# Optimization experiments

Measured on AMD Instinct MI355X. Metric: run time of the kernel, lower is better.

The kernel has to match this reference:

```python
import jax, jax.numpy as jnp
import numpy as np


def setup_inputs() -> dict:
    key = jax.random.key(0)
    k1, k2 = jax.random.split(key)
    B, N, M, D = 4, 8192, 8192, 3
    pred_points = jax.random.normal(k1, (B, N, D), dtype=jnp.float32)
    gt_points = jax.random.normal(k2, (B, M, D), dtype=jnp.float32)
    return {"pred_points": pred_points, "gt_points": gt_points}


def reference(pred_points, gt_points):
    p2 = jnp.sum(pred_points * pred_points, axis=-1)  # [B, N]
    g2 = jnp.sum(gt_points * gt_points, axis=-1)      # [B, M]
    cross = jnp.einsum("bnd,bmd->bnm", pred_points, gt_points)  # [B, N, M]
    d2 = p2[:, :, None] + g2[:, None, :] - 2.0 * cross
    dist = jnp.sqrt(jnp.maximum(d2, 0.0))             # [B, N, M]
    min_pred_to_gt = jnp.min(dist, axis=-1)           # [B, N]
    min_gt_to_pred = jnp.min(dist, axis=-2)           # [B, M]
    return min_pred_to_gt.mean() + min_gt_to_pred.mean()
```

## Files before the change

### kernel.cpp

```cpp
#include <hip/hip_runtime.h>


#define B_ 4
#define N_ 8192
#define TM 1024
#define SM (N_ / TM)
#define THREADS 512
#define CSN 8

__device__ __forceinline__ float min3f(float a, float b, float c) {
  float d;
  asm("v_min3_f32 %0, %1, %2, %3" : "=v"(d) : "v"(a), "v"(b), "v"(c));
  return d;
}

template<int RC>
__global__ __launch_bounds__(THREADS) void chamfer_sym(
    const float* __restrict__ pred, const float* __restrict__ gt,
    float* __restrict__ rowpart, float* __restrict__ colpart,
    float* __restrict__ accws) {
  constexpr int TN = RC * 64;
  constexpr int SN = N_ / TN;
  __shared__ float4 mlds[TM];
  __shared__ float sbuf[4096];

  const int b  = blockIdx.z;
  const int tn = blockIdx.y;
  const int tm = blockIdx.x;
  const int tid = threadIdx.x;
  const int i = tid & 15;
  const int j = tid >> 4;

  if (tm == 0 && tn == 0 && b == 0 && tid == 0) {
    atomicExch(&accws[0], 0.0f);
    atomicExch(((unsigned int*)accws) + 1, 0u);
  }

  const float* qsrc = pred + (size_t)b * N_ * 3;
  const float* tsrc = gt   + (size_t)b * N_ * 3;

  if (tid < 256) {
    const float* tb = tsrc + (size_t)tm * TM * 3;
    const int p0 = tid * 4;
    const float4 f0 = *(const float4*)(tb + 3 * p0);
    const float4 f1 = *(const float4*)(tb + 3 * p0 + 4);
    const float4 f2 = *(const float4*)(tb + 3 * p0 + 8);
    mlds[p0+0] = make_float4(f0.x,f0.y,f0.z, fmaf(f0.x,f0.x,fmaf(f0.y,f0.y,f0.z*f0.z)));
    mlds[p0+1] = make_float4(f0.w,f1.x,f1.y, fmaf(f0.w,f0.w,fmaf(f1.x,f1.x,f1.y*f1.y)));
    mlds[p0+2] = make_float4(f1.z,f1.w,f2.x, fmaf(f1.z,f1.z,fmaf(f1.w,f1.w,f2.x*f2.x)));
    mlds[p0+3] = make_float4(f2.y,f2.z,f2.w, fmaf(f2.y,f2.y,fmaf(f2.z,f2.z,f2.w*f2.w)));
  }

  float colacc[32];
#pragma unroll
  for (int c = 0; c < 32; ++c) colacc[c] = 3.4e38f;

  __syncthreads();

  const int nbase = tn * TN;

  for (int rc = 0; rc < RC; ++rc) {
    const float* qb = qsrc + (size_t)(nbase + rc * 64 + i * 4) * 3;
    const float4 g0 = *(const float4*)(qb);
    const float4 g1 = *(const float4*)(qb + 4);
    const float4 g2 = *(const float4*)(qb + 8);
    const float qx[4] = {g0.x, g0.w, g1.z, g2.y};
    const float qy[4] = {g0.y, g1.x, g1.w, g2.z};
    const float qz[4] = {g0.z, g1.y, g2.x, g2.w};
    float nx[4], ny[4], nz[4], q2[4], racc[4];
#pragma unroll
    for (int r = 0; r < 4; ++r) {
      nx[r] = -2.0f * qx[r]; ny[r] = -2.0f * qy[r]; nz[r] = -2.0f * qz[r];
      q2[r] = fmaf(qx[r],qx[r], fmaf(qy[r],qy[r], qz[r]*qz[r]));
      racc[r] = 3.4e38f;
    }

#pragma unroll
    for (int cs = 0; cs < CSN; ++cs) {
      const int mb = cs * 128 + j * 4;
      const float4 t0 = mlds[mb+0];
      const float4 t1 = mlds[mb+1];
      const float4 t2 = mlds[mb+2];
      const float4 t3 = mlds[mb+3];
      float s[4][4];
#pragma unroll
      for (int r = 0; r < 4; ++r) {
        s[r][0] = fmaf(nx[r],t0.x, fmaf(ny[r],t0.y, fmaf(nz[r],t0.z, t0.w)));
        s[r][1] = fmaf(nx[r],t1.x, fmaf(ny[r],t1.y, fmaf(nz[r],t1.z, t1.w)));
        s[r][2] = fmaf(nx[r],t2.x, fmaf(ny[r],t2.y, fmaf(nz[r],t2.z, t2.w)));
        s[r][3] = fmaf(nx[r],t3.x, fmaf(ny[r],t3.y, fmaf(nz[r],t3.z, t3.w)));
        racc[r] = min3f(racc[r], s[r][0], s[r][1]);
        racc[r] = min3f(racc[r], s[r][2], s[r][3]);
      }
#pragma unroll
      for (int c = 0; c < 4; ++c) {
        colacc[cs*4+c] = min3f(colacc[cs*4+c], s[0][c] + q2[0], s[1][c] + q2[1]);
        colacc[cs*4+c] = min3f(colacc[cs*4+c], s[2][c] + q2[2], s[3][c] + q2[3]);
      }
    }

    const int buf = (rc & 1) * 2048;
#pragma unroll
    for (int r = 0; r < 4; ++r) sbuf[buf + j*64 + i*4 + r] = racc[r] + q2[r];
    __syncthreads();
    {
      const int row = tid >> 3, g = tid & 7;
      const float v0 = sbuf[buf + (g*4+0)*64 + row];
      const float v1 = sbuf[buf + (g*4+1)*64 + row];
      const float v2 = sbuf[buf + (g*4+2)*64 + row];
      const float v3 = sbuf[buf + (g*4+3)*64 + row];
      float v = fminf(min3f(v0, v1, v2), v3);
      v = fminf(v, __shfl_xor(v, 1, 64));
      v = fminf(v, __shfl_xor(v, 2, 64));
      v = fminf(v, __shfl_xor(v, 4, 64));
      if (g == 0)
        rowpart[((size_t)b * SM + tm) * N_ + nbase + rc*64 + row] = v;
    }
  }

  __syncthreads();
#pragma unroll
  for (int p = 0; p < 4; ++p) {
#pragma unroll
    for (int k = 0; k < 8; ++k) {
      sbuf[i*256 + (k>>2)*128 + j*4 + (k&3)] = colacc[(2*p + (k>>2))*4 + (k&3)];
    }
    __syncthreads();
    if (tid < 256) {
      float v = sbuf[tid];
#pragma unroll
      for (int ii = 1; ii <= 13; ii += 2)
        v = min3f(v, sbuf[ii*256 + tid], sbuf[(ii+1)*256 + tid]);
      v = fminf(v, sbuf[15*256 + tid]);
      colpart[((size_t)b * SN + tn) * N_ + tm*TM + p*256 + tid] = v;
    }
    __syncthreads();
  }
}

template<int SN>
__global__ __launch_bounds__(256) void chamfer_fin(
    const float* __restrict__ rowpart, const float* __restrict__ colpart,
    float* __restrict__ accws, float* __restrict__ out) {
  const int t = blockIdx.x * 256 + threadIdx.x;
  const int b = t >> 13;
  const int n = t & (N_ - 1);
  float v = rowpart[(size_t)(b * SM) * N_ + n];
#pragma unroll
  for (int s = 1; s < SM; ++s) v = fminf(v, rowpart[(size_t)(b*SM + s) * N_ + n]);
  float sum = sqrtf(fmaxf(v, 0.0f));
  float w = colpart[(size_t)(b * SN) * N_ + n];
#pragma unroll
  for (int s = 1; s < SN; ++s) w = fminf(w, colpart[(size_t)(b*SN + s) * N_ + n]);
  sum += sqrtf(fmaxf(w, 0.0f));
#pragma unroll
  for (int off = 32; off > 0; off >>= 1) sum += __shfl_down(sum, off, 64);
  __shared__ float ws4[4];
  const int lane = threadIdx.x & 63, wid = threadIdx.x >> 6;
  if (lane == 0) ws4[wid] = sum;
  __syncthreads();
  if (threadIdx.x == 0) {
    const float bs = (ws4[0] + ws4[1]) + (ws4[2] + ws4[3]);
    atomicAdd(&accws[0], bs);
    __threadfence();
    const unsigned old = atomicAdd(((unsigned int*)accws) + 1, 1u);
    if (old == gridDim.x - 1) {
      __threadfence();
      const float tot = atomicAdd(&accws[0], 0.0f);
      out[0] = tot * (1.0f / 32768.0f);
    }
  }
}

extern "C" void kernel_launch(void* const* d_in, const int* in_sizes, int n_in,
                              void* d_out, int out_size, void* d_ws, size_t ws_size,
                              hipStream_t stream) {
  const float* pred = (const float*)d_in[0];
  const float* gt   = (const float*)d_in[1];
  float* out = (float*)d_out;
  float* rowpart = (float*)d_ws;
  const size_t rowfl = (size_t)B_ * SM * N_;
  const size_t base = rowfl * sizeof(float) + 64;

#define LAUNCH(RCV)                                                            \
  {                                                                            \
    constexpr int SNV = N_ / (RCV * 64);                                       \
    float* colpart = rowpart + rowfl;                                          \
    float* accws = colpart + (size_t)B_ * SNV * N_;                            \
    chamfer_sym<RCV><<<dim3(SM, SNV, B_), THREADS, 0, stream>>>(               \
        pred, gt, rowpart, colpart, accws);                                    \
    chamfer_fin<SNV><<<128, 256, 0, stream>>>(rowpart, colpart, accws, out);   \
  }

  if      (ws_size >= base + (size_t)B_ * 8 * N_ * sizeof(float)) LAUNCH(16)
  else if (ws_size >= base + (size_t)B_ * 4 * N_ * sizeof(float)) LAUNCH(32)
  else if (ws_size >= base + (size_t)B_ * 2 * N_ * sizeof(float)) LAUNCH(64)
  else                                                            LAUNCH(128)
#undef LAUNCH
}
```

Baseline: 103.2 us.

## Restructure chamfer kernel with wave-shuffle row reduction and LDS atomicMin column merge

Remaps threads so each wave's 32 lanes cover the column tile, letting row minima be reduced with xor shuffles instead of a shared-memory transpose and extra barriers per row chunk. Column minima are merged with LDS atomicMin on non-negative float bit patterns rather than a multi-pass shared buffer reduction. The mlds layout is XOR-swizzled to avoid bank conflicts, launch bounds are raised to four blocks, RC becomes a runtime parameter with smaller values (more blocks) when workspace allows, and the finisher splits row and column work across threads. Risks include LDS atomic contention and a non-unrolled runtime-RC loop.

```diff
diff --git a/kernel.cpp b/kernel.cpp
--- a/kernel.cpp
+++ b/kernel.cpp
@@ -6,7 +6,7 @@
 #define TM 1024
 #define SM (N_ / TM)
 #define THREADS 512
-#define CSN 8
+#define INF32 3.4e38f
 
 __device__ __forceinline__ float min3f(float a, float b, float c) {
   float d;
@@ -14,53 +14,61 @@
   return d;
 }
 
-template<int RC>
-__global__ __launch_bounds__(THREADS) void chamfer_sym(
+__global__ __launch_bounds__(THREADS, 4) void chamfer_sym(
     const float* __restrict__ pred, const float* __restrict__ gt,
-    float* __restrict__ rowpart, float* __restrict__ colpart,
-    float* __restrict__ accws) {
-  constexpr int TN = RC * 64;
-  constexpr int SN = N_ / TN;
+    float* __restrict__ rowpart, unsigned* __restrict__ colpart,
+    float* __restrict__ accws, int RC) {
   __shared__ float4 mlds[TM];
-  __shared__ float sbuf[4096];
-
-  const int b  = blockIdx.z;
-  const int tn = blockIdx.y;
-  const int tm = blockIdx.x;
+  __shared__ unsigned colbuf[TM];
+
+  const int b = blockIdx.z, tn = blockIdx.y, tm = blockIdx.x;
   const int tid = threadIdx.x;
-  const int i = tid & 15;
-  const int j = tid >> 4;
-
-  if (tm == 0 && tn == 0 && b == 0 && tid == 0) {
-    atomicExch(&accws[0], 0.0f);
-    atomicExch(((unsigned int*)accws) + 1, 0u);
+  const int j = tid & 31;
+  const int iq = tid >> 5;
+  const int SN = gridDim.y;
+  const int TN = N_ / SN;
+
+  if (b == 0 && tn == 0 && tm == 0 && tid == 0) {
+    accws[0] = 0.0f;
+    ((unsigned*)accws)[1] = 0u;
   }
 
   const float* qsrc = pred + (size_t)b * N_ * 3;
-  const float* tsrc = gt   + (size_t)b * N_ * 3;
+  const float* tsrc = gt + (size_t)b * N_ * 3;
 
   if (tid < 256) {
-    const float* tb = tsrc + (size_t)tm * TM * 3;
-    const int p0 = tid * 4;
-    const float4 f0 = *(const float4*)(tb + 3 * p0);
-    const float4 f1 = *(const float4*)(tb + 3 * p0 + 4);
-    const float4 f2 = *(const float4*)(tb + 3 * p0 + 8);
-    mlds[p0+0] = make_float4(f0.x,f0.y,f0.z, fmaf(f0.x,f0.x,fmaf(f0.y,f0.y,f0.z*f0.z)));
-    mlds[p0+1] = make_float4(f0.w,f1.x,f1.y, fmaf(f0.w,f0.w,fmaf(f1.x,f1.x,f1.y*f1.y)));
-    mlds[p0+2] = make_float4(f1.z,f1.w,f2.x, fmaf(f1.z,f1.z,fmaf(f1.w,f1.w,f2.x*f2.x)));
-    mlds[p0+3] = make_float4(f2.y,f2.z,f2.w, fmaf(f2.y,f2.y,fmaf(f2.z,f2.z,f2.w*f2.w)));
+    const float* tb = tsrc + (size_t)tm * TM * 3 + tid * 12;
+    const float4 f0 = *(const float4*)(tb);
+    const float4 f1 = *(const float4*)(tb + 4);
+    const float4 f2 = *(const float4*)(tb + 8);
+    float4 P0 = make_float4(f0.x, f0.y, f0.z, fmaf(f0.x,f0.x, fmaf(f0.y,f0.y, f0.z*f0.z)));
+    float4 P1 = make_float4(f0.w, f1.x, f1.y, fmaf(f0.w,f0.w, fmaf(f1.x,f1.x, f1.y*f1.y)));
+    float4 P2 = make_float4(f1.z, f1.w, f2.x, fmaf(f1.z,f1.z, fmaf(f1.w,f1.w, f2.x*f2.x)));
+    float4 P3 = make_float4(f2.y, f2.z, f2.w, fmaf(f2.y,f2.y, fmaf(f2.z,f2.z, f2.w*f2.w)));
+    const int s = (tid >> 3) & 3;
+    const int base = tid * 4;
+    mlds[base + (0 ^ s)] = P0;
+    mlds[base + (1 ^ s)] = P1;
+    mlds[base + (2 ^ s)] = P2;
+    mlds[base + (3 ^ s)] = P3;
+    ((uint4*)colbuf)[tid] = make_uint4(0x7F7FFFFFu, 0x7F7FFFFFu, 0x7F7FFFFFu, 0x7F7FFFFFu);
   }
 
   float colacc[32];
 #pragma unroll
-  for (int c = 0; c < 32; ++c) colacc[c] = 3.4e38f;
+  for (int c = 0; c < 32; ++c) colacc[c] = INF32;
 
   __syncthreads();
 
-  const int nbase = tn * TN;
+  const int sw = (j >> 3) & 3;
+  const int a0 = 4 * j + (0 ^ sw);
+  const int a1 = 4 * j + (1 ^ sw);
+  const int a2 = 4 * j + (2 ^ sw);
+  const int a3 = 4 * j + (3 ^ sw);
 
   for (int rc = 0; rc < RC; ++rc) {
-    const float* qb = qsrc + (size_t)(nbase + rc * 64 + i * 4) * 3;
+    const int r0 = tn * TN + rc * 64 + iq * 4;
+    const float* qb = qsrc + (size_t)r0 * 3;
     const float4 g0 = *(const float4*)(qb);
     const float4 g1 = *(const float4*)(qb + 4);
     const float4 g2 = *(const float4*)(qb + 8);
@@ -71,88 +79,85 @@
 #pragma unroll
     for (int r = 0; r < 4; ++r) {
       nx[r] = -2.0f * qx[r]; ny[r] = -2.0f * qy[r]; nz[r] = -2.0f * qz[r];
-      q2[r] = fmaf(qx[r],qx[r], fmaf(qy[r],qy[r], qz[r]*qz[r]));
-      racc[r] = 3.4e38f;
-    }
-
-#pragma unroll
-    for (int cs = 0; cs < CSN; ++cs) {
-      const int mb = cs * 128 + j * 4;
-      const float4 t0 = mlds[mb+0];
-      const float4 t1 = mlds[mb+1];
-      const float4 t2 = mlds[mb+2];
-      const float4 t3 = mlds[mb+3];
-      float s[4][4];
+      q2[r] = fmaf(qx[r], qx[r], fmaf(qy[r], qy[r], qz[r] * qz[r]));
+      racc[r] = INF32;
+    }
+
+#pragma unroll
+    for (int cs = 0; cs < 8; ++cs) {
+      const float4 t0 = mlds[cs * 128 + a0];
+      const float4 t1 = mlds[cs * 128 + a1];
+      const float4 t2 = mlds[cs * 128 + a2];
+      const float4 t3 = mlds[cs * 128 + a3];
+      float sc[4][4];
 #pragma unroll
       for (int r = 0; r < 4; ++r) {
-        s[r][0] = fmaf(nx[r],t0.x, fmaf(ny[r],t0.y, fmaf(nz[r],t0.z, t0.w)));
-        s[r][1] = fmaf(nx[r],t1.x, fmaf(ny[r],t1.y, fmaf(nz[r],t1.z, t1.w)));
-        s[r][2] = fmaf(nx[r],t2.x, fmaf(ny[r],t2.y, fmaf(nz[r],t2.z, t2.w)));
-        s[r][3] = fmaf(nx[r],t3.x, fmaf(ny[r],t3.y, fmaf(nz[r],t3.z, t3.w)));
-        racc[r] = min3f(racc[r], s[r][0], s[r][1]);
-        racc[r] = min3f(racc[r], s[r][2], s[r][3]);
+        sc[r][0] = fmaf(nx[r], t0.x, fmaf(ny[r], t0.y, fmaf(nz[r], t0.z, t0.w)));
+        sc[r][1] = fmaf(nx[r], t1.x, fmaf(ny[r], t1.y, fmaf(nz[r], t1.z, t1.w)));
+        sc[r][2] = fmaf(nx[r], t2.x, fmaf(ny[r], t2.y, fmaf(nz[r], t2.z, t2.w)));
+        sc[r][3] = fmaf(nx[r], t3.x, fmaf(ny[r], t3.y, fmaf(nz[r], t3.z, t3.w)));
+        racc[r] = min3f(racc[r], sc[r][0], sc[r][1]);
+        racc[r] = min3f(racc[r], sc[r][2], sc[r][3]);
       }
 #pragma unroll
       for (int c = 0; c < 4; ++c) {
-        colacc[cs*4+c] = min3f(colacc[cs*4+c], s[0][c] + q2[0], s[1][c] + q2[1]);
-        colacc[cs*4+c] = min3f(colacc[cs*4+c], s[2][c] + q2[2], s[3][c] + q2[3]);
+        colacc[cs*4+c] = min3f(colacc[cs*4+c], sc[0][c] + q2[0], sc[1][c] + q2[1]);
+        colacc[cs*4+c] = min3f(colacc[cs*4+c], sc[2][c] + q2[2], sc[3][c] + q2[3]);
       }
     }
 
-    const int buf = (rc & 1) * 2048;
-#pragma unroll
-    for (int r = 0; r < 4; ++r) sbuf[buf + j*64 + i*4 + r] = racc[r] + q2[r];
-    __syncthreads();
-    {
-      const int row = tid >> 3, g = tid & 7;
-      const float v0 = sbuf[buf + (g*4+0)*64 + row];
-      const float v1 = sbuf[buf + (g*4+1)*64 + row];
-      const float v2 = sbuf[buf + (g*4+2)*64 + row];
-      const float v3 = sbuf[buf + (g*4+3)*64 + row];
-      float v = fminf(min3f(v0, v1, v2), v3);
-      v = fminf(v, __shfl_xor(v, 1, 64));
-      v = fminf(v, __shfl_xor(v, 2, 64));
-      v = fminf(v, __shfl_xor(v, 4, 64));
-      if (g == 0)
-        rowpart[((size_t)b * SM + tm) * N_ + nbase + rc*64 + row] = v;
-    }
-  }
-
+#pragma unroll
+    for (int m = 1; m <= 16; m <<= 1) {
+#pragma unroll
+      for (int r = 0; r < 4; ++r)
+        racc[r] = fminf(racc[r], __shfl_xor(racc[r], m, 64));
+    }
+    if (j == 0) {
+      float4 v = make_float4(racc[0] + q2[0], racc[1] + q2[1],
+                             racc[2] + q2[2], racc[3] + q2[3]);
+      *(float4*)&rowpart[((size_t)b * SM + tm) * N_ + r0] = v;
+    }
+  }
+
+#pragma unroll
+  for (int c = 0; c < 32; ++c)
+    colacc[c] = fminf(colacc[c], __shfl_xor(colacc[c], 32, 64));
+  if ((tid & 32) == 0) {
+#pragma unroll
+    for (int cs = 0; cs < 8; ++cs)
+#pragma unroll
+      for (int c = 0; c < 4; ++c)
+        atomicMin(&colbuf[cs * 128 + 4 * j + c],
+                  __float_as_uint(fmaxf(colacc[cs*4+c], 0.0f)));
+  }
   __syncthreads();
-#pragma unroll
-  for (int p = 0; p < 4; ++p) {
-#pragma unroll
-    for (int k = 0; k < 8; ++k) {
-      sbuf[i*256 + (k>>2)*128 + j*4 + (k&3)] = colacc[(2*p + (k>>2))*4 + (k&3)];
-    }
-    __syncthreads();
-    if (tid < 256) {
-      float v = sbuf[tid];
-#pragma unroll
-      for (int ii = 1; ii <= 13; ii += 2)
-        v = min3f(v, sbuf[ii*256 + tid], sbuf[(ii+1)*256 + tid]);
-      v = fminf(v, sbuf[15*256 + tid]);
-      colpart[((size_t)b * SN + tn) * N_ + tm*TM + p*256 + tid] = v;
-    }
-    __syncthreads();
-  }
-}
-
-template<int SN>
+  {
+    unsigned* dst = colpart + ((size_t)b * SN + tn) * N_ + tm * TM;
+    dst[tid] = colbuf[tid];
+    dst[tid + 512] = colbuf[tid + 512];
+  }
+}
+
 __global__ __launch_bounds__(256) void chamfer_fin(
-    const float* __restrict__ rowpart, const float* __restrict__ colpart,
-    float* __restrict__ accws, float* __restrict__ out) {
+    const float* __restrict__ rowpart, const unsigned* __restrict__ colpart,
+    float* __restrict__ accws, float* __restrict__ out, int SN) {
   const int t = blockIdx.x * 256 + threadIdx.x;
-  const int b = t >> 13;
-  const int n = t & (N_ - 1);
-  float v = rowpart[(size_t)(b * SM) * N_ + n];
-#pragma unroll
-  for (int s = 1; s < SM; ++s) v = fminf(v, rowpart[(size_t)(b*SM + s) * N_ + n]);
+  float v;
+  if (t < 32768) {
+    const int b = t >> 13, n = t & (N_ - 1);
+    const float* p = rowpart + (size_t)b * SM * N_ + n;
+    v = p[0];
+#pragma unroll
+    for (int s2 = 1; s2 < SM; ++s2) v = fminf(v, p[(size_t)s2 * N_]);
+  } else {
+    const int u = t - 32768;
+    const int b = u >> 13, n = u & (N_ - 1);
+    const unsigned* p = colpart + (size_t)b * SN * N_ + n;
+    unsigned m = p[0];
+    for (int s2 = 1; s2 < SN; ++s2) m = min(m, p[(size_t)s2 * N_]);
+    v = __uint_as_float(m);
+  }
   float sum = sqrtf(fmaxf(v, 0.0f));
-  float w = colpart[(size_t)(b * SN) * N_ + n];
-#pragma unroll
-  for (int s = 1; s < SN; ++s) w = fminf(w, colpart[(size_t)(b*SN + s) * N_ + n]);
-  sum += sqrtf(fmaxf(w, 0.0f));
 #pragma unroll
   for (int off = 32; off > 0; off >>= 1) sum += __shfl_down(sum, off, 64);
   __shared__ float ws4[4];
@@ -163,7 +168,7 @@
     const float bs = (ws4[0] + ws4[1]) + (ws4[2] + ws4[3]);
     atomicAdd(&accws[0], bs);
     __threadfence();
-    const unsigned old = atomicAdd(((unsigned int*)accws) + 1, 1u);
+    const unsigned old = atomicAdd(((unsigned*)accws) + 1, 1u);
     if (old == gridDim.x - 1) {
       __threadfence();
       const float tot = atomicAdd(&accws[0], 0.0f);
@@ -178,23 +183,18 @@
   const float* pred = (const float*)d_in[0];
   const float* gt   = (const float*)d_in[1];
   float* out = (float*)d_out;
-  float* rowpart = (float*)d_ws;
-  const size_t rowfl = (size_t)B_ * SM * N_;
-  const size_t base = rowfl * sizeof(float) + 64;
-
-#define LAUNCH(RCV)                                                            \
-  {                                                                            \
-    constexpr int SNV = N_ / (RCV * 64);                                       \
-    float* colpart = rowpart + rowfl;                                          \
-    float* accws = colpart + (size_t)B_ * SNV * N_;                            \
-    chamfer_sym<RCV><<<dim3(SM, SNV, B_), THREADS, 0, stream>>>(               \
-        pred, gt, rowpart, colpart, accws);                                    \
-    chamfer_fin<SNV><<<128, 256, 0, stream>>>(rowpart, colpart, accws, out);   \
-  }
-
-  if      (ws_size >= base + (size_t)B_ * 8 * N_ * sizeof(float)) LAUNCH(16)
-  else if (ws_size >= base + (size_t)B_ * 4 * N_ * sizeof(float)) LAUNCH(32)
-  else if (ws_size >= base + (size_t)B_ * 2 * N_ * sizeof(float)) LAUNCH(64)
-  else                                                            LAUNCH(128)
-#undef LAUNCH
-}
+
+  float* accws = (float*)d_ws;
+  float* rowpart = (float*)((char*)d_ws + 64);
+  unsigned* colpart = (unsigned*)(rowpart + (size_t)B_ * SM * N_);
+
+  const size_t base = 64 + (size_t)B_ * SM * N_ * 4;
+  int RC = 16;
+  if (ws_size >= base + (size_t)B_ * 32 * N_ * 4) RC = 4;
+  else if (ws_size >= base + (size_t)B_ * 16 * N_ * 4) RC = 8;
+  const int SN = N_ / (RC * 64);
+
+  chamfer_sym<<<dim3(SM, SN, B_), THREADS, 0, stream>>>(
+      pred, gt, rowpart, colpart, accws, RC);
+  chamfer_fin<<<256, 256, 0, stream>>>(rowpart, colpart, accws, out, SN);
+}
```

New measurement: 104.8 us. Within noise of the previous version (+1.6%).
